# Kernel tuning notes

Measured on AMD Instinct MI355X. Metric: run time of the kernel, lower is better.

## Reference

```python
import jax, jax.numpy as jnp
import numpy as np


def setup_inputs() -> dict:
    key = jax.random.key(0)
    k1, k2, k3, k4 = jax.random.split(key, 4)
    H = W = 1024
    B = 16
    image = jax.random.normal(k1, (1, H, W), dtype=jnp.float32)
    x = jax.random.normal(k2, (B, 1, H, W), dtype=jnp.float32)
    # Conv2d(1, 9, 3) parameters, torch layout: weight (out=9, in=1, 3, 3), bias (9,)
    fan_in = 1 * 3 * 3
    bound = 1.0 / np.sqrt(fan_in)
    W_KL = jax.random.uniform(k3, (9, 1, 3, 3), jnp.float32, -bound, bound)
    b_KL = jax.random.uniform(k4, (9,), jnp.float32, -bound, bound)
    return {"image": image, "x": x, "W_KL": W_KL, "b_KL": b_KL}


def reference(image, x, W_KL, b_KL):
    # K = Conv2d(image): (1,H,W) -> (9,H,W), 'same' padding
    K = jax.lax.conv_general_dilated(
        image[None], W_KL, window_strides=(1, 1), padding='SAME',
        dimension_numbers=('NCHW', 'OIHW', 'NCHW'))[0] + b_KL[:, None, None]
    H, W = image.shape[1], image.shape[2]
    # permute (9,H,W) -> (H,W,9) -> unflatten to per-pixel 3x3 kernels (H,W,3,3)
    K = jnp.transpose(K, (1, 2, 0)).reshape(H, W, 3, 3)
    # Apply spatially-varying 3x3 kernel: y[b,c,h,w] = sum_{a,d} K[h,w,a,d] * x_pad[b,c,h+a,w+d]
    x_pad = jnp.pad(x, ((0, 0), (0, 0), (1, 1), (1, 1)))
    y = jnp.zeros_like(x)
    for a in range(3):
        for d in range(3):
            y = y + K[:, :, a, d] * x_pad[:, :, a:a + H, d:d + W]
    return y
```

## Files before the change

kernel.cpp:

```cpp
#include <hip/hip_runtime.h>

#define IH 1024
#define IW 1024
#define NB 16
#define BPB 4

typedef float v4f __attribute__((ext_vector_type(4)));

struct RawWin { v4f mv[3]; float fl[3]; float fr[3]; };

__device__ __forceinline__ void issue_win(const float* __restrict__ plane,
                                          int h, int w0, RawWin& rw) {
#pragma unroll
    for (int a = 0; a < 3; ++a) {
        const int hh = h + a - 1;
        const int hc = (hh < 0) ? 0 : (hh >= IH ? IH - 1 : hh);
        const float* rowp = plane + (size_t)hc * IW;
        rw.fl[a] = rowp[w0 > 0 ? w0 - 1 : 0];
        rw.mv[a] = *(const v4f*)(rowp + w0);
        rw.fr[a] = rowp[w0 + 4 < IW ? w0 + 4 : IW - 1];
    }
}

__device__ __forceinline__ void fin_win_x(const RawWin& rw, int w0, float win[3][6]) {
#pragma unroll
    for (int a = 0; a < 3; ++a) {
        win[a][0] = (w0 > 0)      ? rw.fl[a]   : 0.f;
        win[a][1] = rw.mv[a].x;
        win[a][2] = rw.mv[a].y;
        win[a][3] = rw.mv[a].z;
        win[a][4] = rw.mv[a].w;
        win[a][5] = (w0 + 4 < IW) ? rw.fr[a]   : 0.f;
    }
}

__device__ __forceinline__ void fin_win_img(const RawWin& rw, int h, int w0,
                                            float win[3][6]) {
#pragma unroll
    for (int a = 0; a < 3; ++a) {
        const int hh = h + a - 1;
        const bool rowok = (hh >= 0) & (hh < IH);
        win[a][0] = (rowok && w0 > 0)      ? rw.fl[a]   : 0.f;
        win[a][1] = rowok ? rw.mv[a].x : 0.f;
        win[a][2] = rowok ? rw.mv[a].y : 0.f;
        win[a][3] = rowok ? rw.mv[a].z : 0.f;
        win[a][4] = rowok ? rw.mv[a].w : 0.f;
        win[a][5] = (rowok && w0 + 4 < IW) ? rw.fr[a]   : 0.f;
    }
}

__global__ __launch_bounds__(256) void fused_smblock(
    const float* __restrict__ image,
    const float* __restrict__ x,
    const float* __restrict__ Wk,
    const float* __restrict__ bk,
    float* __restrict__ out)
{
    const int tx = threadIdx.x;
    const int ty = threadIdx.y;
    const int w0 = blockIdx.x * 256 + tx * 4;
    const int h  = blockIdx.y * 4 + ty;
    const int b0 = blockIdx.z * BPB;

    float wk[81];
#pragma unroll
    for (int i = 0; i < 81; ++i) wk[i] = Wk[i];
    float bb[9];
#pragma unroll
    for (int c = 0; c < 9; ++c) bb[c] = bk[c];

    const size_t plane = (size_t)IH * IW;
    const float* __restrict__ xb = x + (size_t)b0 * plane;

    RawWin rimg;
    issue_win(image, h, w0, rimg);
    RawWin rx[BPB];
#pragma unroll
    for (int i = 0; i < BPB; ++i)
        issue_win(xb + (size_t)i * plane, h, w0, rx[i]);
    __builtin_amdgcn_sched_barrier(0);

    float p[3][6];
    fin_win_img(rimg, h, w0, p);
    float Kv[4][9];
#pragma unroll
    for (int j = 0; j < 4; ++j)
#pragma unroll
        for (int c = 0; c < 9; ++c) {
            float acc = bb[c];
#pragma unroll
            for (int a = 0; a < 3; ++a)
#pragma unroll
                for (int d = 0; d < 3; ++d)
                    acc = fmaf(wk[c * 9 + a * 3 + d], p[a][j + d], acc);
            Kv[j][c] = acc;
        }

    {
        const bool top = (h == 0);
        const bool bot = (h == IH - 1);
#pragma unroll
        for (int j = 0; j < 4; ++j)
#pragma unroll
            for (int d = 0; d < 3; ++d) {
                Kv[j][d]     = top ? 0.f : Kv[j][d];
                Kv[j][6 + d] = bot ? 0.f : Kv[j][6 + d];
            }
    }

    float* __restrict__ ob = out + (size_t)b0 * plane + (size_t)h * IW + w0;
#pragma unroll
    for (int i = 0; i < BPB; ++i) {
        float win[3][6];
        fin_win_x(rx[i], w0, win);
        v4f y;
#pragma unroll
        for (int j = 0; j < 4; ++j) {
            float acc = 0.f;
#pragma unroll
            for (int a = 0; a < 3; ++a)
#pragma unroll
                for (int d = 0; d < 3; ++d)
                    acc = fmaf(Kv[j][a * 3 + d], win[a][j + d], acc);
            y[j] = acc;
        }
        __builtin_nontemporal_store(y, (v4f*)(ob + (size_t)i * plane));
    }
}

extern "C" void kernel_launch(void* const* d_in, const int* in_sizes, int n_in,
                              void* d_out, int out_size, void* d_ws, size_t ws_size,
                              hipStream_t stream) {
    const float* image = (const float*)d_in[0];
    const float* x     = (const float*)d_in[1];
    const float* Wk    = (const float*)d_in[2];
    const float* bk    = (const float*)d_in[3];
    float* out = (float*)d_out;

    dim3 block(64, 4);
    dim3 grid(IW / 256, IH / 4, NB / BPB);
    fused_smblock<<<grid, block, 0, stream>>>(image, x, Wk, bk, out);
}
```

Before: 141.3 us.

## Stage x row windows in LDS via direct global-to-LDS loads

Replaces per-thread register loads of the 3-row x windows (including scalar halo loads) with async global_load_lds 16-byte copies into a shared buffer holding full rows for 4 batches. Each block now covers one full image row per batch group, and neighbours' halo values are read from LDS. This removes the redundant scalar halo global loads. In exchange it uses 48KB of LDS per block, which limits occupancy, and needs a barrier before compute.

```diff
diff --git a/kernel.cpp b/kernel.cpp
--- a/kernel.cpp
+++ b/kernel.cpp
@@ -1,4 +1,5 @@
 #include <hip/hip_runtime.h>
+#include <stdint.h>
 
 #define IH 1024
 #define IW 1024
@@ -6,6 +7,12 @@
 #define BPB 4
 
 typedef float v4f __attribute__((ext_vector_type(4)));
+
+__device__ __forceinline__ void glds16(const float* g, float* l) {
+    __builtin_amdgcn_global_load_lds(
+        (const __attribute__((address_space(1))) void*)g,
+        (__attribute__((address_space(3))) void*)l, 16, 0, 0);
+}
 
 struct RawWin { v4f mv[3]; float fl[3]; float fr[3]; };
 
@@ -19,18 +26,6 @@
         rw.fl[a] = rowp[w0 > 0 ? w0 - 1 : 0];
         rw.mv[a] = *(const v4f*)(rowp + w0);
         rw.fr[a] = rowp[w0 + 4 < IW ? w0 + 4 : IW - 1];
-    }
-}
-
-__device__ __forceinline__ void fin_win_x(const RawWin& rw, int w0, float win[3][6]) {
-#pragma unroll
-    for (int a = 0; a < 3; ++a) {
-        win[a][0] = (w0 > 0)      ? rw.fl[a]   : 0.f;
-        win[a][1] = rw.mv[a].x;
-        win[a][2] = rw.mv[a].y;
-        win[a][3] = rw.mv[a].z;
-        win[a][4] = rw.mv[a].w;
-        win[a][5] = (w0 + 4 < IW) ? rw.fr[a]   : 0.f;
     }
 }
 
@@ -49,18 +44,39 @@
     }
 }
 
-__global__ __launch_bounds__(256) void fused_smblock(
+__global__ __launch_bounds__(256) void fused_lds(
     const float* __restrict__ image,
     const float* __restrict__ x,
     const float* __restrict__ Wk,
     const float* __restrict__ bk,
     float* __restrict__ out)
 {
-    const int tx = threadIdx.x;
-    const int ty = threadIdx.y;
-    const int w0 = blockIdx.x * 256 + tx * 4;
-    const int h  = blockIdx.y * 4 + ty;
-    const int b0 = blockIdx.z * BPB;
+    __shared__ float lds[BPB][3][IW];
+
+    const int tid  = threadIdx.x;
+    const int lane = tid & 63;
+    const int wv   = tid >> 6;
+    const int h    = blockIdx.x;
+    const int b0   = blockIdx.y * BPB;
+    const int w0   = tid * 4;
+
+    const size_t plane = (size_t)IH * IW;
+    const float* __restrict__ xb = x + (size_t)b0 * plane;
+
+    RawWin rimg;
+    issue_win(image, h, w0, rimg);
+
+    const int qoff = wv * 256 + lane * 4;
+#pragma unroll
+    for (int b = 0; b < BPB; ++b)
+#pragma unroll
+        for (int a = 0; a < 3; ++a) {
+            const int hh = h + a - 1;
+            const int hc = (hh < 0) ? 0 : (hh >= IH ? IH - 1 : hh);
+            glds16(xb + (size_t)b * plane + (size_t)hc * IW + qoff,
+                   &lds[b][a][wv * 256]);
+        }
+    __builtin_amdgcn_sched_barrier(0);
 
     float wk[81];
 #pragma unroll
@@ -68,17 +84,6 @@
     float bb[9];
 #pragma unroll
     for (int c = 0; c < 9; ++c) bb[c] = bk[c];
-
-    const size_t plane = (size_t)IH * IW;
-    const float* __restrict__ xb = x + (size_t)b0 * plane;
-
-    RawWin rimg;
-    issue_win(image, h, w0, rimg);
-    RawWin rx[BPB];
-#pragma unroll
-    for (int i = 0; i < BPB; ++i)
-        issue_win(xb + (size_t)i * plane, h, w0, rx[i]);
-    __builtin_amdgcn_sched_barrier(0);
 
     float p[3][6];
     fin_win_img(rimg, h, w0, p);
@@ -108,11 +113,27 @@
             }
     }
 
+    asm volatile("s_waitcnt vmcnt(0)" ::: "memory");
+    __syncthreads();
+
     float* __restrict__ ob = out + (size_t)b0 * plane + (size_t)h * IW + w0;
+    const int wl = (w0 >= 4) ? w0 - 4 : 0;
+    const int wr = (w0 + 4 < IW) ? w0 + 4 : IW - 4;
 #pragma unroll
-    for (int i = 0; i < BPB; ++i) {
+    for (int b = 0; b < BPB; ++b) {
         float win[3][6];
-        fin_win_x(rx[i], w0, win);
+#pragma unroll
+        for (int a = 0; a < 3; ++a) {
+            const v4f lv = *(const v4f*)&lds[b][a][wl];
+            const v4f mv = *(const v4f*)&lds[b][a][w0];
+            const v4f rv = *(const v4f*)&lds[b][a][wr];
+            win[a][0] = (w0 > 0)      ? lv.w : 0.f;
+            win[a][1] = mv.x;
+            win[a][2] = mv.y;
+            win[a][3] = mv.z;
+            win[a][4] = mv.w;
+            win[a][5] = (w0 + 4 < IW) ? rv.x : 0.f;
+        }
         v4f y;
 #pragma unroll
         for (int j = 0; j < 4; ++j) {
@@ -124,7 +145,7 @@
                     acc = fmaf(Kv[j][a * 3 + d], win[a][j + d], acc);
             y[j] = acc;
         }
-        __builtin_nontemporal_store(y, (v4f*)(ob + (size_t)i * plane));
+        __builtin_nontemporal_store(y, (v4f*)(ob + (size_t)b * plane));
     }
 }
 
@@ -137,7 +158,7 @@
     const float* bk    = (const float*)d_in[3];
     float* out = (float*)d_out;
 
-    dim3 block(64, 4);
-    dim3 grid(IW / 256, IH / 4, NB / BPB);
-    fused_smblock<<<grid, block, 0, stream>>>(image, x, Wk, bk, out);
+    dim3 block(256);
+    dim3 grid(IH, NB / BPB);
+    fused_lds<<<grid, block, 0, stream>>>(image, x, Wk, bk, out);
 }
```

After: 142.5 us. Within noise of the previous version (+0.8%).

## Double-buffer x tiles through LDS with async global_load_lds across all batches

Applied to the files above, without the earlier changes.

Each block now covers all 16 batches for a 4-row by 256-column tile, so the per-pixel kernel K is computed once instead of once per batch group. The x row tiles, including the vertical halo, are staged into a double-buffered LDS array with global_load_lds while the previous batch is computed, and horizontal halo values are loaded separately. Block indices are remapped so each XCD gets contiguous rows. The aims are to remove redundant image loads and K recomputation and to overlap loads with compute. The cost is hand-written vmcnt waits and a barrier per batch, whose correctness and effect depend on the order in which memory operations are issued.

```diff
diff --git a/kernel.cpp b/kernel.cpp
--- a/kernel.cpp
+++ b/kernel.cpp
@@ -3,9 +3,14 @@
 #define IH 1024
 #define IW 1024
 #define NB 16
-#define BPB 4
 
 typedef float v4f __attribute__((ext_vector_type(4)));
+
+__device__ __forceinline__ void glds16(const float* g, float* l) {
+    __builtin_amdgcn_global_load_lds(
+        (const __attribute__((address_space(1))) void*)g,
+        (__attribute__((address_space(3))) void*)l, 16, 0, 0);
+}
 
 struct RawWin { v4f mv[3]; float fl[3]; float fr[3]; };
 
@@ -19,18 +24,6 @@
         rw.fl[a] = rowp[w0 > 0 ? w0 - 1 : 0];
         rw.mv[a] = *(const v4f*)(rowp + w0);
         rw.fr[a] = rowp[w0 + 4 < IW ? w0 + 4 : IW - 1];
-    }
-}
-
-__device__ __forceinline__ void fin_win_x(const RawWin& rw, int w0, float win[3][6]) {
-#pragma unroll
-    for (int a = 0; a < 3; ++a) {
-        win[a][0] = (w0 > 0)      ? rw.fl[a]   : 0.f;
-        win[a][1] = rw.mv[a].x;
-        win[a][2] = rw.mv[a].y;
-        win[a][3] = rw.mv[a].z;
-        win[a][4] = rw.mv[a].w;
-        win[a][5] = (w0 + 4 < IW) ? rw.fr[a]   : 0.f;
     }
 }
 
@@ -49,36 +42,67 @@
     }
 }
 
-__global__ __launch_bounds__(256) void fused_smblock(
+__global__ __launch_bounds__(256, 4) void fused_dbuf(
     const float* __restrict__ image,
     const float* __restrict__ x,
     const float* __restrict__ Wk,
     const float* __restrict__ bk,
     float* __restrict__ out)
 {
+    __shared__ float lds[2][6][256];
+
     const int tx = threadIdx.x;
-    const int ty = threadIdx.y;
-    const int w0 = blockIdx.x * 256 + tx * 4;
-    const int h  = blockIdx.y * 4 + ty;
-    const int b0 = blockIdx.z * BPB;
-
-    float wk[81];
-#pragma unroll
-    for (int i = 0; i < 81; ++i) wk[i] = Wk[i];
-    float bb[9];
-#pragma unroll
-    for (int c = 0; c < 9; ++c) bb[c] = bk[c];
+    const int wv = threadIdx.y;
+
+    const int hwid  = blockIdx.x;
+    const int xcd   = hwid & 7;
+    const int chunk = hwid >> 3;
+    const int bx    = chunk & 3;
+    const int g     = xcd * 32 + (chunk >> 2);
+    const int c0    = bx * 256;
+    const int h0    = g * 4;
+    const int h     = h0 + wv;
+    const int lc    = tx * 4;
+    const int w0    = c0 + lc;
 
     const size_t plane = (size_t)IH * IW;
-    const float* __restrict__ xb = x + (size_t)b0 * plane;
+
+    int zv; asm("v_mov_b32 %0, 0" : "=v"(zv));
+
+    auto stage = [&](int b, int buf) {
+        const float* xb = x + (size_t)b * plane;
+        int gr = h0 - 1 + wv; gr = gr < 0 ? 0 : gr;
+        glds16(xb + (size_t)gr * IW + c0 + tx * 4, &lds[buf][wv][0]);
+        if (wv < 2) {
+            int g2 = h0 + 3 + wv; g2 = g2 > IH - 1 ? IH - 1 : g2;
+            glds16(xb + (size_t)g2 * IW + c0 + tx * 4, &lds[buf][wv + 4][0]);
+        }
+    };
+    auto halo = [&](int b, float* HL, float* HR) {
+        const float* xb = x + (size_t)b * plane;
+        const int cl = (c0 > 0) ? c0 - 1 : 0;
+        const int cr = (c0 + 256 < IW) ? c0 + 256 : IW - 1;
+#pragma unroll
+        for (int a = 0; a < 3; ++a) {
+            int gr = h + a - 1; gr = gr < 0 ? 0 : (gr > IH - 1 ? IH - 1 : gr);
+            const float* rp = xb + (size_t)gr * IW;
+            HL[a] = rp[cl + zv];
+            HR[a] = rp[cr + zv];
+        }
+    };
 
     RawWin rimg;
     issue_win(image, h, w0, rimg);
-    RawWin rx[BPB];
-#pragma unroll
-    for (int i = 0; i < BPB; ++i)
-        issue_win(xb + (size_t)i * plane, h, w0, rx[i]);
-    __builtin_amdgcn_sched_barrier(0);
+    stage(0, 0);
+    float hl[2][3], hr[2][3];
+    halo(0, hl[0], hr[0]);
+
+    float wkk[81];
+#pragma unroll
+    for (int i = 0; i < 81; ++i) wkk[i] = Wk[i];
+    float bb[9];
+#pragma unroll
+    for (int c = 0; c < 9; ++c) bb[c] = bk[c];
 
     float p[3][6];
     fin_win_img(rimg, h, w0, p);
@@ -92,10 +116,9 @@
             for (int a = 0; a < 3; ++a)
 #pragma unroll
                 for (int d = 0; d < 3; ++d)
-                    acc = fmaf(wk[c * 9 + a * 3 + d], p[a][j + d], acc);
+                    acc = fmaf(wkk[c * 9 + a * 3 + d], p[a][j + d], acc);
             Kv[j][c] = acc;
         }
-
     {
         const bool top = (h == 0);
         const bool bot = (h == IH - 1);
@@ -108,24 +131,63 @@
             }
     }
 
-    float* __restrict__ ob = out + (size_t)b0 * plane + (size_t)h * IW + w0;
-#pragma unroll
-    for (int i = 0; i < BPB; ++i) {
-        float win[3][6];
-        fin_win_x(rx[i], w0, win);
-        v4f y;
-#pragma unroll
-        for (int j = 0; j < 4; ++j) {
-            float acc = 0.f;
-#pragma unroll
-            for (int a = 0; a < 3; ++a)
-#pragma unroll
-                for (int d = 0; d < 3; ++d)
-                    acc = fmaf(Kv[j][a * 3 + d], win[a][j + d], acc);
-            y[j] = acc;
-        }
-        __builtin_nontemporal_store(y, (v4f*)(ob + (size_t)i * plane));
-    }
+    asm volatile("s_waitcnt vmcnt(6)" ::: "memory");
+    __builtin_amdgcn_sched_barrier(0);
+    __builtin_amdgcn_s_barrier();
+    __builtin_amdgcn_sched_barrier(0);
+
+    v4f yv[2];
+    float* obp = out + (size_t)h * IW + w0;
+
+#pragma unroll
+    for (int b = 0; b < NB; ++b) {
+        if (b > 0)
+            __builtin_nontemporal_store(yv[(b - 1) & 1],
+                                        (v4f*)(obp + (size_t)(b - 1) * plane));
+        if (b + 1 < NB) {
+            stage(b + 1, (b + 1) & 1);
+            halo(b + 1, hl[(b + 1) & 1], hr[(b + 1) & 1]);
+        }
+        {
+            const int ll = (tx > 0)  ? lc - 4 : 0;
+            const int lr = (tx < 63) ? lc + 4 : 252;
+            const float* lb = &lds[b & 1][0][0];
+            float win[3][6];
+#pragma unroll
+            for (int a = 0; a < 3; ++a) {
+                const float* rowp = lb + (wv + a) * 256;
+                const v4f lv = *(const v4f*)(rowp + ll);
+                const v4f mv = *(const v4f*)(rowp + lc);
+                const v4f rv = *(const v4f*)(rowp + lr);
+                const float le = (tx == 0)  ? hl[b & 1][a] : lv.w;
+                const float re = (tx == 63) ? hr[b & 1][a] : rv.x;
+                win[a][0] = (w0 > 0)      ? le : 0.f;
+                win[a][1] = mv.x; win[a][2] = mv.y;
+                win[a][3] = mv.z; win[a][4] = mv.w;
+                win[a][5] = (w0 + 4 < IW) ? re : 0.f;
+            }
+            v4f yy;
+#pragma unroll
+            for (int j = 0; j < 4; ++j) {
+                float acc = 0.f;
+#pragma unroll
+                for (int a = 0; a < 3; ++a)
+#pragma unroll
+                    for (int d = 0; d < 3; ++d)
+                        acc = fmaf(Kv[j][a * 3 + d], win[a][j + d], acc);
+                yy[j] = acc;
+            }
+            yv[b & 1] = yy;
+        }
+        if (b + 1 < NB) {
+            asm volatile("s_waitcnt vmcnt(6)" ::: "memory");
+            __builtin_amdgcn_sched_barrier(0);
+            __builtin_amdgcn_s_barrier();
+            __builtin_amdgcn_sched_barrier(0);
+        }
+    }
+    __builtin_nontemporal_store(yv[(NB - 1) & 1],
+                                (v4f*)(obp + (size_t)(NB - 1) * plane));
 }
 
 extern "C" void kernel_launch(void* const* d_in, const int* in_sizes, int n_in,
@@ -138,6 +200,6 @@
     float* out = (float*)d_out;
 
     dim3 block(64, 4);
-    dim3 grid(IW / 256, IH / 4, NB / BPB);
-    fused_smblock<<<grid, block, 0, stream>>>(image, x, Wk, bk, out);
-}
+    dim3 grid(1024);
+    fused_dbuf<<<grid, block, 0, stream>>>(image, x, Wk, bk, out);
+}
```

Result: faster. 123.9 us (-12.3%).
